# Kernel optimization log

Hardware: AMD Instinct MI355X
Metric: run time of the kernel (lower is better)

Reference implementation:

```python
import jax, jax.numpy as jnp
import numpy as np

B, S, H, D, M = 4, 512, 768, 24, 96
OUT_HID = 2 * max(128, H // 2)  # 768

def setup_inputs() -> dict:
    key = jax.random.key(0)
    ks = jax.random.split(key, 10)
    g = lambda k, shp, s=0.02: (jax.random.normal(k, shp, jnp.float32) * s)
    return {
        'H_j': jax.random.normal(ks[0], (B, S, H), jnp.float32),
        'H_i': jax.random.normal(ks[1], (B, S, H), jnp.float32),
        'attn_mask': jnp.ones((B, S), jnp.float32),
        'p_j_w': g(ks[2], (D, H)),
        'p_i_w': g(ks[3], (D, H)),
        's_w1': g(ks[4], (M, 4 * D)),
        's_b1': jnp.zeros((M,), jnp.float32),
        's_w2': g(ks[5], (1, M)),
        's_b2': jnp.zeros((1,), jnp.float32),
        'v_w1': g(ks[6], (OUT_HID, 3 * H)),
        'v_b1': jnp.zeros((OUT_HID,), jnp.float32),
        'v_w2': g(ks[7], (H, OUT_HID)),
        'v_b2': jnp.zeros((H,), jnp.float32),
        'alpha': jnp.asarray(0.05, jnp.float32),
    }

def reference(H_j, H_i, attn_mask, p_j_w, p_i_w, s_w1, s_b1, s_w2, s_b2,
              v_w1, v_b1, v_w2, v_b2, alpha):
    # Projections: [B,S,D]
    Zj = H_j @ p_j_w.T
    Zi = H_i @ p_i_w.T
    # score_mlp layer1 on concat([Zj_pair, Zi_pair, hadam, |diff|]) ==
    # sum of the 4 block-matmuls (block-split of W1 over the concat axis).
    Wa, Wb, Wc, Wd = jnp.split(s_w1, 4, axis=1)        # each [M, D]
    Zj_p = Zj[:, :, None, :]                            # [B,S,1,D]
    Zi_p = Zi[:, None, :, :]                            # [B,1,S,D]
    hid = (jnp.einsum('bsd,md->bsm', Zj, Wa)[:, :, None, :]
           + jnp.einsum('btd,md->btm', Zi, Wb)[:, None, :, :]
           + jnp.einsum('bstd,md->bstm', Zj_p * Zi_p, Wc)
           + jnp.einsum('bstd,md->bstm', jnp.abs(Zj_p - Zi_p), Wd)
           + s_b1)                                      # [B,S,S,M]
    logits = jnp.einsum('bstm,om->bst', jax.nn.relu(hid), s_w2)[..., :] + s_b2[0]  # [B,S,S]
    neg = jnp.finfo(logits.dtype).min
    logits = logits + (1.0 - attn_mask)[:, None, :] * neg  # mask over keys
    probs = jax.nn.softmax(logits, axis=-1)
    ctx = jnp.einsum('bst,bth->bsh', probs, H_i)           # [B,S,H]
    msg_in = jnp.concatenate([ctx, H_j, ctx * H_j], axis=-1)  # concat_hadam: [B,S,3H]
    msg = jax.nn.relu(msg_in @ v_w1.T + v_b1) @ v_w2.T + v_b2
    return alpha * msg  # dropout is identity in eval mode
```

## Files before the change

### kernel.cpp

```cpp
#include <hip/hip_runtime.h>
#include <hip/hip_bf16.h>
#include <math.h>

#define BB 4
#define SS 512
#define HH 768
#define DD 24
#define MM 96
#define OH 768
#define K3H 2304

typedef unsigned short u16;
typedef unsigned int u32;
typedef short bf16x8 __attribute__((ext_vector_type(8)));
typedef float f32x4 __attribute__((ext_vector_type(4)));
typedef u16 u16x4 __attribute__((ext_vector_type(4)));

#define MB_MSGIN  0
#define MB_H1     (MB_MSGIN + BB*SS*K3H)
#define MB_W1     (MB_H1    + BB*SS*OH)
#define MB_W2     (MB_W1    + OH*K3H)
#define MB_PROBS  (MB_W2    + OH*HH)
#define MB_HIT    (MB_PROBS + BB*SS*SS)
#define MB_ZJP    (MB_HIT   + BB*HH*SS)
#define MB_ZIP    (MB_ZJP   + BB*SS*32)
#define MB_WM     (MB_ZIP   + BB*SS*32)
#define MB_WAB    (MB_WM    + MM*96)
#define MB_AB     (MB_WAB   + MM*32)

__device__ inline u16 f2bf(float x) {
    union { float f; u32 u; } v; v.f = x;
    u32 r = v.u + 0x7fffu + ((v.u >> 16) & 1u);
    return (u16)(r >> 16);
}
__device__ inline u32 pk2bf(float lo, float hi) {
    return ((__float_as_uint(lo) + 0x8000u) >> 16) |
           ((__float_as_uint(hi) + 0x8000u) & 0xffff0000u);
}
__device__ inline void unpack8(bf16x8 v, float* f) {
    const u32* d = (const u32*)&v;
    #pragma unroll
    for (int i = 0; i < 4; ++i) {
        f[2*i]   = __uint_as_float(d[i] << 16);
        f[2*i+1] = __uint_as_float(d[i] & 0xffff0000u);
    }
}
__device__ inline void gl_lds16(const u16* g, u16* l) {
    __builtin_amdgcn_global_load_lds(
        (const __attribute__((address_space(1))) void*)g,
        (__attribute__((address_space(3))) void*)l, 16, 0, 0);
}
__device__ inline bf16x8 frag64(const u16* X, int r, int g) {
    return *(const bf16x8*)&X[(r*8 + (g ^ (r & 7)))*8];
}

__global__ __launch_bounds__(256) void k_wprep(
    const float* __restrict__ sw1, const float* __restrict__ vw1,
    const float* __restrict__ vw2,
    u16* __restrict__ Wm, u16* __restrict__ Wab,
    u16* __restrict__ w1b, u16* __restrict__ w2b)
{
    int bx = blockIdx.x;
    if (bx == 0) {
        for (int i = threadIdx.x; i < MM*96; i += 256) {
            int m = i / 96, k = i % 96;
            float v = 0.f;
            if (k < 24)                 v = sw1[m*96 + 48 + k];
            else if (k >= 32 && k < 56) v = sw1[m*96 + 72 + (k - 32)];
            else if (k >= 64 && k < 88) v = sw1[m*96 + 24 + (k - 64)];
            Wm[i] = f2bf(v);
        }
        for (int i = threadIdx.x; i < MM*32; i += 256) {
            int m = i >> 5, k = i & 31;
            Wab[i] = (k < 24) ? f2bf(sw1[m*96 + k]) : (u16)0;
        }
        return;
    }
    int idx = bx - 1;
    const float* src; u16* dst;
    if (idx < 864) { src = vw1; dst = w1b; }
    else           { idx -= 864; src = vw2; dst = w2b; }
    int i = (idx*256 + threadIdx.x) * 8;
    float4 a = *(const float4*)&src[i];
    float4 c = *(const float4*)&src[i+4];
    u16x4 lo = { f2bf(a.x), f2bf(a.y), f2bf(a.z), f2bf(a.w) };
    u16x4 hi = { f2bf(c.x), f2bf(c.y), f2bf(c.z), f2bf(c.w) };
    *(u16x4*)&dst[i]   = lo;
    *(u16x4*)&dst[i+4] = hi;
}

__global__ __launch_bounds__(256) void k_zgemm(
    const float* __restrict__ Hj, const float* __restrict__ Hi,
    const float* __restrict__ pjw, const float* __restrict__ piw,
    const float* __restrict__ sw1, const float* __restrict__ sb1,
    const u16* __restrict__ Wab,
    u16* __restrict__ Zjp, u16* __restrict__ Zip, u16* __restrict__ Ab)
{
    int isJ = (blockIdx.y == 0);
    const float* H = isJ ? Hj : Hi;
    const float* P = isJ ? pjw : piw;
    u16* Zout = isJ ? Zjp : Zip;
    int n0 = blockIdx.x * 64;
    int tid = threadIdx.x, wave = tid >> 6, lane = tid & 63;
    int q = lane >> 4, l16 = lane & 15;
    __shared__ __align__(16) u16 As[64*32];
    __shared__ __align__(16) u16 Bs[32*32];
    __shared__ __align__(16) u16 zb[64*32];

    { int i = tid; Bs[(24 + (i >> 5))*32 + (i & 31)] = 0; }

    int arow = tid >> 2, aseg = tid & 3;
    const float* ah = H + (size_t)(n0 + arow)*HH + aseg*8;
    int brow = tid >> 2, bseg = tid & 3;
    const float* bh = P + (size_t)brow*HH + bseg*8;
    int adst = arow*32 + ((aseg ^ (arow & 3))*8);
    int bdst = brow*32 + ((bseg ^ (brow & 3))*8);

    float4 xa = *(const float4*)(ah);
    float4 ya = *(const float4*)(ah + 4);
    float4 xb = {}, yb = {};
    if (tid < 96) { xb = *(const float4*)(bh); yb = *(const float4*)(bh + 4); }

    f32x4 acc0 = {}, acc1 = {};
    int ga = q ^ (l16 & 3);
    for (int k0 = 0; k0 < HH; k0 += 32) {
        { u32* w = (u32*)&As[adst];
          w[0] = pk2bf(xa.x, xa.y); w[1] = pk2bf(xa.z, xa.w);
          w[2] = pk2bf(ya.x, ya.y); w[3] = pk2bf(ya.z, ya.w); }
        if (tid < 96) {
          u32* w = (u32*)&Bs[bdst];
          w[0] = pk2bf(xb.x, xb.y); w[1] = pk2bf(xb.z, xb.w);
          w[2] = pk2bf(yb.x, yb.y); w[3] = pk2bf(yb.z, yb.w); }
        float4 nxa = {}, nya = {}, nxb = {}, nyb = {};
        if (k0 + 32 < HH) {
            nxa = *(const float4*)(ah + k0 + 32);
            nya = *(const float4*)(ah + k0 + 36);
            if (tid < 96) { nxb = *(const float4*)(bh + k0 + 32);
                            nyb = *(const float4*)(bh + k0 + 36); }
        }
        __syncthreads();
        bf16x8 af = *(const bf16x8*)&As[(wave*16 + l16)*32 + ga*8];
        bf16x8 b0 = *(const bf16x8*)&Bs[l16*32 + ga*8];
        bf16x8 b1 = *(const bf16x8*)&Bs[(16 + l16)*32 + ga*8];
        acc0 = __builtin_amdgcn_mfma_f32_16x16x32_bf16(af, b0, acc0, 0,0,0);
        acc1 = __builtin_amdgcn_mfma_f32_16x16x32_bf16(af, b1, acc1, 0,0,0);
        __syncthreads();
        xa = nxa; ya = nya; xb = nxb; yb = nyb;
    }
    #pragma unroll
    for (int r = 0; r < 4; ++r) {
        zb[(wave*16 + q*4 + r)*32 + l16]      = f2bf(acc0[r]);
        zb[(wave*16 + q*4 + r)*32 + 16 + l16] = f2bf(acc1[r]);
    }
    __syncthreads();
    { uint4 v = *(const uint4*)&zb[tid*8];
      *(uint4*)&Zout[(size_t)n0*32 + tid*8] = v; }
    if (isJ) {
        bf16x8 af = *(const bf16x8*)&zb[(wave*16 + l16)*32 + q*8];
        #pragma unroll
        for (int nt = 0; nt < 6; ++nt) {
            bf16x8 bw = *(const bf16x8*)&Wab[(nt*16 + l16)*32 + q*8];
            f32x4 a = {};
            a = __builtin_amdgcn_mfma_f32_16x16x32_bf16(af, bw, a, 0,0,0);
            float bv = sb1[nt*16 + l16];
            #pragma unroll
            for (int r = 0; r < 4; ++r) {
                int bs = n0 + wave*16 + q*4 + r;
                Ab[(size_t)bs*MM + nt*16 + l16] = f2bf(a[r] + bv);
            }
        }
    }
}

__global__ __launch_bounds__(256) void k_pair_mfma(
    const u16* __restrict__ Zjp, const u16* __restrict__ Zip,
    const u16* __restrict__ Ab, const u16* __restrict__ Wm,
    const float* __restrict__ sw2, const float* __restrict__ mask,
    u16* __restrict__ probsb)
{
    int blk = blockIdx.x; int b = blk >> 8; int s0 = (blk & 255) * 2;
    int tid = threadIdx.x, wave = tid >> 6, lane = tid & 63;
    int q = lane >> 4, l16 = lane & 15;
    int si = wave & 1, half = wave >> 1;
    int s = s0 + si, bs = b*SS + s;
    __shared__ __align__(16) u16 ZiS[SS*32];
    __shared__ float logits[2][SS];

    {
        const u16* zb = Zip + (size_t)b*SS*32;
        #pragma unroll
        for (int p = 0; p < 8; ++p) {
            int idx = p*256 + tid;
            int t = idx >> 2, c = idx & 3;
            int g = c ^ ((t + (t >> 2)) & 3);
            gl_lds16(zb + t*32 + g*8, ZiS + idx*8);
        }
    }

    bf16x8 zjf = *(const bf16x8*)&Zjp[(size_t)bs*32 + q*8];
    float zj[8]; unpack8(zjf, zj);
    bf16x8 afc[6], afd[6];
    #pragma unroll
    for (int mt = 0; mt < 6; ++mt) {
        const u16* wrow = &Wm[(mt*16 + l16)*96];
        bf16x8 wcf = *(const bf16x8*)&wrow[q*8];
        afd[mt]    = *(const bf16x8*)&wrow[32 + q*8];
        bf16x8 wbf = *(const bf16x8*)&wrow[64 + q*8];
        float fc[8], fb[8];
        unpack8(wcf, fc); unpack8(wbf, fb);
        u32 aval = (u32)Ab[(size_t)bs*MM + mt*16 + l16];
        union { u32 d[4]; bf16x8 v; } pk;
        #pragma unroll
        for (int i = 0; i < 4; ++i)
            pk.d[i] = pk2bf(fmaf(fc[2*i], zj[2*i], fb[2*i]),
                            fmaf(fc[2*i+1], zj[2*i+1], fb[2*i+1]));
        pk.d[0] = (q == 3) ? aval : pk.d[0];
        afc[mt] = pk.v;
    }
    float w2v[6][4];
    #pragma unroll
    for (int mt = 0; mt < 6; ++mt)
        #pragma unroll
        for (int r = 0; r < 4; ++r) w2v[mt][r] = sw2[mt*16 + q*4 + r];

    __syncthreads();

    for (int k = 0; k < 16; ++k) {
        int t0 = (half*16 + k) * 16;
        int trow = t0 + l16;
        int sw = q ^ ((trow + (trow >> 2)) & 3);
        bf16x8 zif = *(const bf16x8*)&ZiS[trow*32 + sw*8];
        float zi[8]; unpack8(zif, zi);
        union { u32 d[4]; bf16x8 v; } b1, b2;
        #pragma unroll
        for (int i = 0; i < 4; ++i)
            b1.d[i] = pk2bf(fabsf(zj[2*i] - zi[2*i]), fabsf(zj[2*i+1] - zi[2*i+1]));
        b2.v = zif;
        b2.d[0] = (q == 3) ? 0x3F80u : b2.d[0];
        f32x4 acc[6];
        #pragma unroll
        for (int mt = 0; mt < 6; ++mt) {
            f32x4 a = {};
            a = __builtin_amdgcn_mfma_f32_16x16x32_bf16(afc[mt], b2.v, a, 0,0,0);
            a = __builtin_amdgcn_mfma_f32_16x16x32_bf16(afd[mt], b1.v, a, 0,0,0);
            acc[mt] = a;
        }
        float p = 0.f;
        #pragma unroll
        for (int mt = 0; mt < 6; ++mt)
            #pragma unroll
            for (int r = 0; r < 4; ++r)
                p = fmaf(fmaxf(acc[mt][r], 0.f), w2v[mt][r], p);
        p += __shfl_xor(p, 16);
        p += __shfl_xor(p, 32);
        if (lane < 16) logits[si][t0 + lane] = p;
    }
    __syncthreads();

    if (wave < 2) {
        const float NEGF = -3.4028234663852886e38f;
        int bss = b*SS + s0 + wave;
        float l[8], e[8];
        float mx = -INFINITY;
        #pragma unroll
        for (int i = 0; i < 8; ++i) {
            int idx = lane + i*64;
            l[i] = logits[wave][idx] + (1.f - mask[b*SS + idx]) * NEGF;
            mx = fmaxf(mx, l[i]);
        }
        #pragma unroll
        for (int off = 32; off > 0; off >>= 1) mx = fmaxf(mx, __shfl_xor(mx, off));
        float sum = 0.f;
        #pragma unroll
        for (int i = 0; i < 8; ++i) { e[i] = __expf(l[i] - mx); sum += e[i]; }
        #pragma unroll
        for (int off = 32; off > 0; off >>= 1) sum += __shfl_xor(sum, off);
        float inv = 1.f / sum;
        #pragma unroll
        for (int i = 0; i < 8; ++i)
            probsb[(size_t)bss*SS + lane + i*64] = f2bf(e[i] * inv);
    }
}

__global__ __launch_bounds__(256) void k_hit(
    const float* __restrict__ Hi, u16* __restrict__ HiTb)
{
    int b = blockIdx.z, t0 = blockIdx.x*64, h0 = blockIdx.y*64;
    __shared__ u16 tile[64*74];
    int r = threadIdx.x >> 2, cs = threadIdx.x & 3;
    const float* src = Hi + ((size_t)(b*SS) + t0 + r)*HH + h0 + cs*16;
    u16* dst = &tile[r*74 + cs*16];
    #pragma unroll
    for (int i = 0; i < 4; ++i) {
        float4 v = *(const float4*)(src + i*4);
        *(u32*)&dst[i*4]     = pk2bf(v.x, v.y);
        *(u32*)&dst[i*4 + 2] = pk2bf(v.z, v.w);
    }
    __syncthreads();
    int hr = threadIdx.x >> 2;
    u16 outv[16];
    #pragma unroll
    for (int i = 0; i < 16; ++i) outv[i] = tile[(cs*16 + i)*74 + hr];
    u16* o = HiTb + ((size_t)b*HH + h0 + hr)*SS + t0 + cs*16;
    *(uint4*)o       = *(const uint4*)&outv[0];
    *(uint4*)(o + 8) = *(const uint4*)&outv[8];
}

__global__ __launch_bounds__(256) void k_ctx_mfma(
    const u16* __restrict__ probsb, const u16* __restrict__ HiTb,
    const float* __restrict__ Hj, u16* __restrict__ msginb)
{
    int b = blockIdx.z;
    int h0 = blockIdx.x * 64;
    int s0 = blockIdx.y * 64;
    int tid = threadIdx.x;
    __shared__ __align__(16) u16 As[64*64];
    __shared__ __align__(16) u16 Bs[64*64];
    int wave = tid >> 6, lane = tid & 63;
    int wr = (wave >> 1) * 32, wc = (wave & 1) * 32;
    int q = lane >> 4, l16 = lane & 15;
    f32x4 acc[2][2] = {};
    const u16* ag = probsb + ((size_t)(b*SS) + s0)*SS;
    const u16* bg = HiTb + ((size_t)b*HH + h0)*SS;
    for (int k0 = 0; k0 < SS; k0 += 64) {
        #pragma unroll
        for (int p = 0; p < 2; ++p) {
            int sl = p*256 + tid; int rr = sl >> 3, gi = sl & 7, g = gi ^ (rr & 7);
            gl_lds16(ag + (size_t)rr*SS + k0 + g*8, As + sl*8);
            gl_lds16(bg + (size_t)rr*SS + k0 + g*8, Bs + sl*8);
        }
        __syncthreads();
        #pragma unroll
        for (int ks = 0; ks < 2; ++ks) {
            int g = ks*4 + q;
            bf16x8 a0 = frag64(As, wr + l16, g);
            bf16x8 a1 = frag64(As, wr + 16 + l16, g);
            bf16x8 b0 = frag64(Bs, wc + l16, g);
            bf16x8 b1 = frag64(Bs, wc + 16 + l16, g);
            acc[0][0] = __builtin_amdgcn_mfma_f32_16x16x32_bf16(a0, b0, acc[0][0], 0,0,0);
            acc[0][1] = __builtin_amdgcn_mfma_f32_16x16x32_bf16(a0, b1, acc[0][1], 0,0,0);
            acc[1][0] = __builtin_amdgcn_mfma_f32_16x16x32_bf16(a1, b0, acc[1][0], 0,0,0);
            acc[1][1] = __builtin_amdgcn_mfma_f32_16x16x32_bf16(a1, b1, acc[1][1], 0,0,0);
        }
        __syncthreads();
    }
    #pragma unroll
    for (int rt = 0; rt < 2; ++rt) {
        #pragma unroll
        for (int ct = 0; ct < 2; ++ct) {
            int h = h0 + wc + ct*16 + l16;
            #pragma unroll
            for (int r = 0; r < 4; ++r) {
                int s = s0 + wr + rt*16 + q*4 + r;
                float v = acc[rt][ct][r];
                float hj = Hj[((size_t)(b*SS) + s)*HH + h];
                u16* mb = msginb + (size_t)(b*SS + s)*K3H + h;
                mb[0]    = f2bf(v);
                mb[HH]   = f2bf(hj);
                mb[2*HH] = f2bf(v * hj);
            }
        }
    }
}

__global__ __launch_bounds__(256) void k_mfma_gemm1(
    const u16* __restrict__ Abf, const u16* __restrict__ Bbf,
    const float* __restrict__ bias, u16* __restrict__ Cbf)
{
    int o0 = blockIdx.x * 64;
    int n0 = blockIdx.y * 64;
    int tid = threadIdx.x;
    __shared__ __align__(16) u16 As[64*64];
    __shared__ __align__(16) u16 Bs[64*64];
    int wave = tid >> 6, lane = tid & 63;
    int wr = (wave >> 1) * 32, wc = (wave & 1) * 32;
    int q = lane >> 4, l16 = lane & 15;
    f32x4 acc[2][2] = {};
    const u16* ag = Abf + (size_t)n0*K3H;
    const u16* bg = Bbf + (size_t)o0*K3H;
    for (int k0 = 0; k0 < K3H; k0 += 64) {
        #pragma unroll
        for (int p = 0; p < 2; ++p) {
            int sl = p*256 + tid; int rr = sl >> 3, gi = sl & 7, g = gi ^ (rr & 7);
            gl_lds16(ag + (size_t)rr*K3H + k0 + g*8, As + sl*8);
            gl_lds16(bg + (size_t)rr*K3H + k0 + g*8, Bs + sl*8);
        }
        __syncthreads();
        #pragma unroll
        for (int ks = 0; ks < 2; ++ks) {
            int g = ks*4 + q;
            bf16x8 a0 = frag64(As, wr + l16, g);
            bf16x8 a1 = frag64(As, wr + 16 + l16, g);
            bf16x8 b0 = frag64(Bs, wc + l16, g);
            bf16x8 b1 = frag64(Bs, wc + 16 + l16, g);
            acc[0][0] = __builtin_amdgcn_mfma_f32_16x16x32_bf16(a0, b0, acc[0][0], 0,0,0);
            acc[0][1] = __builtin_amdgcn_mfma_f32_16x16x32_bf16(a0, b1, acc[0][1], 0,0,0);
            acc[1][0] = __builtin_amdgcn_mfma_f32_16x16x32_bf16(a1, b0, acc[1][0], 0,0,0);
            acc[1][1] = __builtin_amdgcn_mfma_f32_16x16x32_bf16(a1, b1, acc[1][1], 0,0,0);
        }
        __syncthreads();
    }
    #pragma unroll
    for (int rt = 0; rt < 2; ++rt) {
        #pragma unroll
        for (int ct = 0; ct < 2; ++ct) {
            int o = o0 + wc + ct*16 + l16;
            float bv = bias[o];
            #pragma unroll
            for (int r = 0; r < 4; ++r) {
                int m = n0 + wr + rt*16 + q*4 + r;
                Cbf[(size_t)m*OH + o] = f2bf(fmaxf(acc[rt][ct][r] + bv, 0.f));
            }
        }
    }
}

__global__ __launch_bounds__(256) void k_mfma_gemm2(
    const u16* __restrict__ Abf, const u16* __restrict__ Bbf,
    const float* __restrict__ bias, const float* __restrict__ alpha,
    float* __restrict__ out)
{
    int o0 = blockIdx.x * 64;
    int n0 = blockIdx.y * 64;
    int tid = threadIdx.x;
    __shared__ __align__(16) u16 As[64*64];
    __shared__ __align__(16) u16 Bs[64*64];
    int wave = tid >> 6, lane = tid & 63;
    int wr = (wave >> 1) * 32, wc = (wave & 1) * 32;
    int q = lane >> 4, l16 = lane & 15;
    f32x4 acc[2][2] = {};
    const u16* ag = Abf + (size_t)n0*OH;
    const u16* bg = Bbf + (size_t)o0*OH;
    for (int k0 = 0; k0 < OH; k0 += 64) {
        #pragma unroll
        for (int p = 0; p < 2; ++p) {
            int sl = p*256 + tid; int rr = sl >> 3, gi = sl & 7, g = gi ^ (rr & 7);
            gl_lds16(ag + (size_t)rr*OH + k0 + g*8, As + sl*8);
            gl_lds16(bg + (size_t)rr*OH + k0 + g*8, Bs + sl*8);
        }
        __syncthreads();
        #pragma unroll
        for (int ks = 0; ks < 2; ++ks) {
            int g = ks*4 + q;
            bf16x8 a0 = frag64(As, wr + l16, g);
            bf16x8 a1 = frag64(As, wr + 16 + l16, g);
            bf16x8 b0 = frag64(Bs, wc + l16, g);
            bf16x8 b1 = frag64(Bs, wc + 16 + l16, g);
            acc[0][0] = __builtin_amdgcn_mfma_f32_16x16x32_bf16(a0, b0, acc[0][0], 0,0,0);
            acc[0][1] = __builtin_amdgcn_mfma_f32_16x16x32_bf16(a0, b1, acc[0][1], 0,0,0);
            acc[1][0] = __builtin_amdgcn_mfma_f32_16x16x32_bf16(a1, b0, acc[1][0], 0,0,0);
            acc[1][1] = __builtin_amdgcn_mfma_f32_16x16x32_bf16(a1, b1, acc[1][1], 0,0,0);
        }
        __syncthreads();
    }
    float al = alpha[0];
    #pragma unroll
    for (int rt = 0; rt < 2; ++rt) {
        #pragma unroll
        for (int ct = 0; ct < 2; ++ct) {
            int o = o0 + wc + ct*16 + l16;
            float bv = bias[o];
            #pragma unroll
            for (int r = 0; r < 4; ++r) {
                int m = n0 + wr + rt*16 + q*4 + r;
                out[(size_t)m*HH + o] = al * (acc[rt][ct][r] + bv);
            }
        }
    }
}

extern "C" void kernel_launch(void* const* d_in, const int* in_sizes, int n_in,
                              void* d_out, int out_size, void* d_ws, size_t ws_size,
                              hipStream_t stream) {
    const float* Hj    = (const float*)d_in[0];
    const float* Hi    = (const float*)d_in[1];
    const float* amask = (const float*)d_in[2];
    const float* pjw   = (const float*)d_in[3];
    const float* piw   = (const float*)d_in[4];
    const float* sw1   = (const float*)d_in[5];
    const float* sb1   = (const float*)d_in[6];
    const float* sw2   = (const float*)d_in[7];
    const float* sb2   = (const float*)d_in[8];
    const float* vw1   = (const float*)d_in[9];
    const float* vb1   = (const float*)d_in[10];
    const float* vw2   = (const float*)d_in[11];
    const float* vb2   = (const float*)d_in[12];
    const float* alpha = (const float*)d_in[13];
    float* out = (float*)d_out;
    (void)sb2;

    u16* bfbase = (u16*)d_ws;
    u16* msginb = bfbase + MB_MSGIN;
    u16* h1b    = bfbase + MB_H1;
    u16* w1b    = bfbase + MB_W1;
    u16* w2b    = bfbase + MB_W2;
    u16* probsb = bfbase + MB_PROBS;
    u16* hitb   = bfbase + MB_HIT;
    u16* zjp    = bfbase + MB_ZJP;
    u16* zip    = bfbase + MB_ZIP;
    u16* wm     = bfbase + MB_WM;
    u16* wab    = bfbase + MB_WAB;
    u16* ab     = bfbase + MB_AB;

    k_wprep<<<1 + 864 + 288, 256, 0, stream>>>(sw1, vw1, vw2, wm, wab, w1b, w2b);
    k_zgemm<<<dim3(32, 2), 256, 0, stream>>>(Hj, Hi, pjw, piw, sw1, sb1, wab, zjp, zip, ab);
    k_hit<<<dim3(SS/64, HH/64, BB), 256, 0, stream>>>(Hi, hitb);
    k_pair_mfma<<<BB*SS/2, 256, 0, stream>>>(zjp, zip, ab, wm, sw2, amask, probsb);
    k_ctx_mfma<<<dim3(HH/64, SS/64, BB), 256, 0, stream>>>(probsb, hitb, Hj, msginb);
    k_mfma_gemm1<<<dim3(OH/64, BB*SS/64), 256, 0, stream>>>(msginb, w1b, vb1, h1b);
    k_mfma_gemm2<<<dim3(HH/64, BB*SS/64), 256, 0, stream>>>(h1b, w2b, vb2, alpha, out);
}
```

Before: 194.5 us.

## Merge prep kernels into one launch and vectorize ctx epilogue via LDS staging

Merges the weight conversion, Z projection GEMM and Hi transpose into one block-indexed prep kernel. The prep kernel now also writes the bf16 copy of Hj into the middle slice of the message input. The context GEMM epilogue stages its accumulators through LDS and writes ctx and ctx*Hj as 16-byte vector stores, reading the bf16 Hj back instead of strided fp32 loads. This cuts kernel launches and scattered 2-byte stores. The product now uses bf16-rounded ctx and Hj, and the small Wm prep remains a separate single-block kernel.

```diff
diff --git a/kernel.cpp b/kernel.cpp
--- a/kernel.cpp
+++ b/kernel.cpp
@@ -54,121 +54,162 @@
     return *(const bf16x8*)&X[(r*8 + (g ^ (r & 7)))*8];
 }
 
-__global__ __launch_bounds__(256) void k_wprep(
-    const float* __restrict__ sw1, const float* __restrict__ vw1,
-    const float* __restrict__ vw2,
-    u16* __restrict__ Wm, u16* __restrict__ Wab,
-    u16* __restrict__ w1b, u16* __restrict__ w2b)
+__global__ __launch_bounds__(256) void k_wm(
+    const float* __restrict__ sw1, u16* __restrict__ Wm, u16* __restrict__ Wab)
 {
-    int bx = blockIdx.x;
-    if (bx == 0) {
-        for (int i = threadIdx.x; i < MM*96; i += 256) {
-            int m = i / 96, k = i % 96;
-            float v = 0.f;
-            if (k < 24)                 v = sw1[m*96 + 48 + k];
-            else if (k >= 32 && k < 56) v = sw1[m*96 + 72 + (k - 32)];
-            else if (k >= 64 && k < 88) v = sw1[m*96 + 24 + (k - 64)];
-            Wm[i] = f2bf(v);
-        }
-        for (int i = threadIdx.x; i < MM*32; i += 256) {
-            int m = i >> 5, k = i & 31;
-            Wab[i] = (k < 24) ? f2bf(sw1[m*96 + k]) : (u16)0;
-        }
-        return;
-    }
-    int idx = bx - 1;
-    const float* src; u16* dst;
-    if (idx < 864) { src = vw1; dst = w1b; }
-    else           { idx -= 864; src = vw2; dst = w2b; }
-    int i = (idx*256 + threadIdx.x) * 8;
-    float4 a = *(const float4*)&src[i];
-    float4 c = *(const float4*)&src[i+4];
-    u16x4 lo = { f2bf(a.x), f2bf(a.y), f2bf(a.z), f2bf(a.w) };
-    u16x4 hi = { f2bf(c.x), f2bf(c.y), f2bf(c.z), f2bf(c.w) };
-    *(u16x4*)&dst[i]   = lo;
-    *(u16x4*)&dst[i+4] = hi;
-}
-
-__global__ __launch_bounds__(256) void k_zgemm(
+    for (int i = threadIdx.x; i < MM*96; i += 256) {
+        int m = i / 96, k = i % 96;
+        float v = 0.f;
+        if (k < 24)                 v = sw1[m*96 + 48 + k];
+        else if (k >= 32 && k < 56) v = sw1[m*96 + 72 + (k - 32)];
+        else if (k >= 64 && k < 88) v = sw1[m*96 + 24 + (k - 64)];
+        Wm[i] = f2bf(v);
+    }
+    for (int i = threadIdx.x; i < MM*32; i += 256) {
+        int m = i >> 5, k = i & 31;
+        Wab[i] = (k < 24) ? f2bf(sw1[m*96 + k]) : (u16)0;
+    }
+}
+
+#define PZ_END   64
+#define PC1_END  928
+#define PC2_END  1216
+#define PHJ_END  1984
+#define PHT_END  2368
+
+__global__ __launch_bounds__(256) void k_prep(
     const float* __restrict__ Hj, const float* __restrict__ Hi,
     const float* __restrict__ pjw, const float* __restrict__ piw,
-    const float* __restrict__ sw1, const float* __restrict__ sb1,
+    const float* __restrict__ sb1,
+    const float* __restrict__ vw1, const float* __restrict__ vw2,
     const u16* __restrict__ Wab,
-    u16* __restrict__ Zjp, u16* __restrict__ Zip, u16* __restrict__ Ab)
+    u16* __restrict__ w1b, u16* __restrict__ w2b,
+    u16* __restrict__ Zjp, u16* __restrict__ Zip, u16* __restrict__ Ab,
+    u16* __restrict__ msginb, u16* __restrict__ HiTb)
 {
-    int isJ = (blockIdx.y == 0);
-    const float* H = isJ ? Hj : Hi;
-    const float* P = isJ ? pjw : piw;
-    u16* Zout = isJ ? Zjp : Zip;
-    int n0 = blockIdx.x * 64;
-    int tid = threadIdx.x, wave = tid >> 6, lane = tid & 63;
-    int q = lane >> 4, l16 = lane & 15;
-    __shared__ __align__(16) u16 As[64*32];
-    __shared__ __align__(16) u16 Bs[32*32];
-    __shared__ __align__(16) u16 zb[64*32];
-
-    { int i = tid; Bs[(24 + (i >> 5))*32 + (i & 31)] = 0; }
-
-    int arow = tid >> 2, aseg = tid & 3;
-    const float* ah = H + (size_t)(n0 + arow)*HH + aseg*8;
-    int brow = tid >> 2, bseg = tid & 3;
-    const float* bh = P + (size_t)brow*HH + bseg*8;
-    int adst = arow*32 + ((aseg ^ (arow & 3))*8);
-    int bdst = brow*32 + ((bseg ^ (brow & 3))*8);
-
-    float4 xa = *(const float4*)(ah);
-    float4 ya = *(const float4*)(ah + 4);
-    float4 xb = {}, yb = {};
-    if (tid < 96) { xb = *(const float4*)(bh); yb = *(const float4*)(bh + 4); }
-
-    f32x4 acc0 = {}, acc1 = {};
-    int ga = q ^ (l16 & 3);
-    for (int k0 = 0; k0 < HH; k0 += 32) {
-        { u32* w = (u32*)&As[adst];
-          w[0] = pk2bf(xa.x, xa.y); w[1] = pk2bf(xa.z, xa.w);
-          w[2] = pk2bf(ya.x, ya.y); w[3] = pk2bf(ya.z, ya.w); }
-        if (tid < 96) {
-          u32* w = (u32*)&Bs[bdst];
-          w[0] = pk2bf(xb.x, xb.y); w[1] = pk2bf(xb.z, xb.w);
-          w[2] = pk2bf(yb.x, yb.y); w[3] = pk2bf(yb.z, yb.w); }
-        float4 nxa = {}, nya = {}, nxb = {}, nyb = {};
-        if (k0 + 32 < HH) {
-            nxa = *(const float4*)(ah + k0 + 32);
-            nya = *(const float4*)(ah + k0 + 36);
-            if (tid < 96) { nxb = *(const float4*)(bh + k0 + 32);
-                            nyb = *(const float4*)(bh + k0 + 36); }
-        }
-        __syncthreads();
-        bf16x8 af = *(const bf16x8*)&As[(wave*16 + l16)*32 + ga*8];
-        bf16x8 b0 = *(const bf16x8*)&Bs[l16*32 + ga*8];
-        bf16x8 b1 = *(const bf16x8*)&Bs[(16 + l16)*32 + ga*8];
-        acc0 = __builtin_amdgcn_mfma_f32_16x16x32_bf16(af, b0, acc0, 0,0,0);
-        acc1 = __builtin_amdgcn_mfma_f32_16x16x32_bf16(af, b1, acc1, 0,0,0);
-        __syncthreads();
-        xa = nxa; ya = nya; xb = nxb; yb = nyb;
-    }
-    #pragma unroll
-    for (int r = 0; r < 4; ++r) {
-        zb[(wave*16 + q*4 + r)*32 + l16]      = f2bf(acc0[r]);
-        zb[(wave*16 + q*4 + r)*32 + 16 + l16] = f2bf(acc1[r]);
-    }
-    __syncthreads();
-    { uint4 v = *(const uint4*)&zb[tid*8];
-      *(uint4*)&Zout[(size_t)n0*32 + tid*8] = v; }
-    if (isJ) {
-        bf16x8 af = *(const bf16x8*)&zb[(wave*16 + l16)*32 + q*8];
-        #pragma unroll
-        for (int nt = 0; nt < 6; ++nt) {
-            bf16x8 bw = *(const bf16x8*)&Wab[(nt*16 + l16)*32 + q*8];
-            f32x4 a = {};
-            a = __builtin_amdgcn_mfma_f32_16x16x32_bf16(af, bw, a, 0,0,0);
-            float bv = sb1[nt*16 + l16];
+    __shared__ __align__(16) u16 smem[5120];
+    int bx = blockIdx.x;
+    int tid = threadIdx.x;
+
+    if (bx < PZ_END) {
+        int idx = bx;
+        int isJ = (idx < 32);
+        int n0 = (idx & 31) * 64;
+        const float* H = isJ ? Hj : Hi;
+        const float* P = isJ ? pjw : piw;
+        u16* Zout = isJ ? Zjp : Zip;
+        u16* As = smem;
+        u16* Bs = smem + 2048;
+        u16* zb = smem + 3072;
+        int wave = tid >> 6, lane = tid & 63;
+        int q = lane >> 4, l16 = lane & 15;
+
+        { int i = tid; Bs[(24 + (i >> 5))*32 + (i & 31)] = 0; }
+
+        int arow = tid >> 2, aseg = tid & 3;
+        const float* ah = H + (size_t)(n0 + arow)*HH + aseg*8;
+        const float* bh = P + (size_t)arow*HH + aseg*8;
+        int adst = arow*32 + ((aseg ^ (arow & 3))*8);
+
+        float4 xa = *(const float4*)(ah);
+        float4 ya = *(const float4*)(ah + 4);
+        float4 xb = {}, yb = {};
+        if (tid < 96) { xb = *(const float4*)(bh); yb = *(const float4*)(bh + 4); }
+
+        f32x4 acc0 = {}, acc1 = {};
+        int ga = q ^ (l16 & 3);
+        for (int k0 = 0; k0 < HH; k0 += 32) {
+            { u32* w = (u32*)&As[adst];
+              w[0] = pk2bf(xa.x, xa.y); w[1] = pk2bf(xa.z, xa.w);
+              w[2] = pk2bf(ya.x, ya.y); w[3] = pk2bf(ya.z, ya.w); }
+            if (tid < 96) {
+              u32* w = (u32*)&Bs[adst];
+              w[0] = pk2bf(xb.x, xb.y); w[1] = pk2bf(xb.z, xb.w);
+              w[2] = pk2bf(yb.x, yb.y); w[3] = pk2bf(yb.z, yb.w); }
+            float4 nxa = {}, nya = {}, nxb = {}, nyb = {};
+            if (k0 + 32 < HH) {
+                nxa = *(const float4*)(ah + k0 + 32);
+                nya = *(const float4*)(ah + k0 + 36);
+                if (tid < 96) { nxb = *(const float4*)(bh + k0 + 32);
+                                nyb = *(const float4*)(bh + k0 + 36); }
+            }
+            __syncthreads();
+            bf16x8 af = *(const bf16x8*)&As[(wave*16 + l16)*32 + ga*8];
+            bf16x8 b0 = *(const bf16x8*)&Bs[l16*32 + ga*8];
+            bf16x8 b1 = *(const bf16x8*)&Bs[(16 + l16)*32 + ga*8];
+            acc0 = __builtin_amdgcn_mfma_f32_16x16x32_bf16(af, b0, acc0, 0,0,0);
+            acc1 = __builtin_amdgcn_mfma_f32_16x16x32_bf16(af, b1, acc1, 0,0,0);
+            __syncthreads();
+            xa = nxa; ya = nya; xb = nxb; yb = nyb;
+        }
+        #pragma unroll
+        for (int r = 0; r < 4; ++r) {
+            zb[(wave*16 + q*4 + r)*32 + l16]      = f2bf(acc0[r]);
+            zb[(wave*16 + q*4 + r)*32 + 16 + l16] = f2bf(acc1[r]);
+        }
+        __syncthreads();
+        { uint4 v = *(const uint4*)&zb[tid*8];
+          *(uint4*)&Zout[(size_t)n0*32 + tid*8] = v; }
+        if (isJ) {
+            bf16x8 af = *(const bf16x8*)&zb[(wave*16 + l16)*32 + q*8];
             #pragma unroll
-            for (int r = 0; r < 4; ++r) {
-                int bs = n0 + wave*16 + q*4 + r;
-                Ab[(size_t)bs*MM + nt*16 + l16] = f2bf(a[r] + bv);
+            for (int nt = 0; nt < 6; ++nt) {
+                bf16x8 bw = *(const bf16x8*)&Wab[(nt*16 + l16)*32 + q*8];
+                f32x4 a = {};
+                a = __builtin_amdgcn_mfma_f32_16x16x32_bf16(af, bw, a, 0,0,0);
+                float bv = sb1[nt*16 + l16];
+                #pragma unroll
+                for (int r = 0; r < 4; ++r) {
+                    int bs = n0 + wave*16 + q*4 + r;
+                    Ab[(size_t)bs*MM + nt*16 + l16] = f2bf(a[r] + bv);
+                }
             }
         }
+    } else if (bx < PC2_END) {
+        int idx; const float* src; u16* dst;
+        if (bx < PC1_END) { idx = bx - PZ_END;  src = vw1; dst = w1b; }
+        else              { idx = bx - PC1_END; src = vw2; dst = w2b; }
+        int i = (idx*256 + tid) * 8;
+        float4 a = *(const float4*)&src[i];
+        float4 c = *(const float4*)&src[i+4];
+        u16x4 lo = { f2bf(a.x), f2bf(a.y), f2bf(a.z), f2bf(a.w) };
+        u16x4 hi = { f2bf(c.x), f2bf(c.y), f2bf(c.z), f2bf(c.w) };
+        *(u16x4*)&dst[i]   = lo;
+        *(u16x4*)&dst[i+4] = hi;
+    } else if (bx < PHJ_END) {
+        int idx = bx - PC2_END;
+        int e = (idx*256 + tid) * 8;
+        int n = e / HH, k = e - n*HH;
+        float4 a = *(const float4*)&Hj[e];
+        float4 c = *(const float4*)&Hj[e+4];
+        u16* dst = msginb + (size_t)n*K3H + HH + k;
+        u16x4 lo = { f2bf(a.x), f2bf(a.y), f2bf(a.z), f2bf(a.w) };
+        u16x4 hi = { f2bf(c.x), f2bf(c.y), f2bf(c.z), f2bf(c.w) };
+        *(u16x4*)&dst[0] = lo;
+        *(u16x4*)&dst[4] = hi;
+    } else {
+        int idx = bx - PHJ_END;
+        int t0 = (idx & 7) * 64;
+        int h0 = ((idx >> 3) % 12) * 64;
+        int b  = idx / 96;
+        u16* tile = smem;
+        int r = tid >> 2, cs = tid & 3;
+        const float* src = Hi + ((size_t)(b*SS) + t0 + r)*HH + h0 + cs*16;
+        u16* dst = &tile[r*74 + cs*16];
+        #pragma unroll
+        for (int i = 0; i < 4; ++i) {
+            float4 v = *(const float4*)(src + i*4);
+            *(u32*)&dst[i*4]     = pk2bf(v.x, v.y);
+            *(u32*)&dst[i*4 + 2] = pk2bf(v.z, v.w);
+        }
+        __syncthreads();
+        int hr = tid >> 2;
+        u16 outv[16];
+        #pragma unroll
+        for (int i = 0; i < 16; ++i) outv[i] = tile[(cs*16 + i)*74 + hr];
+        u16* o = HiTb + ((size_t)b*HH + h0 + hr)*SS + t0 + cs*16;
+        *(uint4*)o       = *(const uint4*)&outv[0];
+        *(uint4*)(o + 8) = *(const uint4*)&outv[8];
     }
 }
 
@@ -282,40 +323,17 @@
     }
 }
 
-__global__ __launch_bounds__(256) void k_hit(
-    const float* __restrict__ Hi, u16* __restrict__ HiTb)
-{
-    int b = blockIdx.z, t0 = blockIdx.x*64, h0 = blockIdx.y*64;
-    __shared__ u16 tile[64*74];
-    int r = threadIdx.x >> 2, cs = threadIdx.x & 3;
-    const float* src = Hi + ((size_t)(b*SS) + t0 + r)*HH + h0 + cs*16;
-    u16* dst = &tile[r*74 + cs*16];
-    #pragma unroll
-    for (int i = 0; i < 4; ++i) {
-        float4 v = *(const float4*)(src + i*4);
-        *(u32*)&dst[i*4]     = pk2bf(v.x, v.y);
-        *(u32*)&dst[i*4 + 2] = pk2bf(v.z, v.w);
-    }
-    __syncthreads();
-    int hr = threadIdx.x >> 2;
-    u16 outv[16];
-    #pragma unroll
-    for (int i = 0; i < 16; ++i) outv[i] = tile[(cs*16 + i)*74 + hr];
-    u16* o = HiTb + ((size_t)b*HH + h0 + hr)*SS + t0 + cs*16;
-    *(uint4*)o       = *(const uint4*)&outv[0];
-    *(uint4*)(o + 8) = *(const uint4*)&outv[8];
-}
-
 __global__ __launch_bounds__(256) void k_ctx_mfma(
     const u16* __restrict__ probsb, const u16* __restrict__ HiTb,
-    const float* __restrict__ Hj, u16* __restrict__ msginb)
+    u16* __restrict__ msginb)
 {
     int b = blockIdx.z;
     int h0 = blockIdx.x * 64;
     int s0 = blockIdx.y * 64;
     int tid = threadIdx.x;
-    __shared__ __align__(16) u16 As[64*64];
-    __shared__ __align__(16) u16 Bs[64*64];
+    __shared__ __align__(16) u16 smem[8192];
+    u16* As = smem;
+    u16* Bs = smem + 4096;
     int wave = tid >> 6, lane = tid & 63;
     int wr = (wave >> 1) * 32, wc = (wave & 1) * 32;
     int q = lane >> 4, l16 = lane & 15;
@@ -344,22 +362,39 @@
         }
         __syncthreads();
     }
+    u16* zb = smem;
     #pragma unroll
-    for (int rt = 0; rt < 2; ++rt) {
+    for (int rt = 0; rt < 2; ++rt)
         #pragma unroll
         for (int ct = 0; ct < 2; ++ct) {
-            int h = h0 + wc + ct*16 + l16;
+            int hl = wc + ct*16 + l16;
             #pragma unroll
-            for (int r = 0; r < 4; ++r) {
-                int s = s0 + wr + rt*16 + q*4 + r;
-                float v = acc[rt][ct][r];
-                float hj = Hj[((size_t)(b*SS) + s)*HH + h];
-                u16* mb = msginb + (size_t)(b*SS + s)*K3H + h;
-                mb[0]    = f2bf(v);
-                mb[HH]   = f2bf(hj);
-                mb[2*HH] = f2bf(v * hj);
-            }
-        }
+            for (int r = 0; r < 4; ++r)
+                zb[(wr + rt*16 + q*4 + r)*72 + hl] = f2bf(acc[rt][ct][r]);
+        }
+    __syncthreads();
+    {
+        int s_l = tid >> 2, seg = tid & 3;
+        u16 cv[16], hv[16], pv[16];
+        *(uint4*)&cv[0] = *(const uint4*)&zb[s_l*72 + seg*16];
+        *(uint4*)&cv[8] = *(const uint4*)&zb[s_l*72 + seg*16 + 8];
+        u16* row = msginb + (size_t)(b*SS + s0 + s_l)*K3H;
+        int hc = h0 + seg*16;
+        *(uint4*)&hv[0] = *(const uint4*)&row[HH + hc];
+        *(uint4*)&hv[8] = *(const uint4*)&row[HH + hc + 8];
+        #pragma unroll
+        for (int i = 0; i < 8; ++i) {
+            float c0 = __uint_as_float((u32)cv[2*i] << 16);
+            float c1 = __uint_as_float((u32)cv[2*i+1] << 16);
+            float g0 = __uint_as_float((u32)hv[2*i] << 16);
+            float g1 = __uint_as_float((u32)hv[2*i+1] << 16);
+            u32 pr = pk2bf(c0*g0, c1*g1);
+            pv[2*i] = (u16)pr; pv[2*i+1] = (u16)(pr >> 16);
+        }
+        *(uint4*)&row[hc]     = *(const uint4*)&cv[0];
+        *(uint4*)&row[hc + 8] = *(const uint4*)&cv[8];
+        *(uint4*)&row[2*HH + hc]     = *(const uint4*)&pv[0];
+        *(uint4*)&row[2*HH + hc + 8] = *(const uint4*)&pv[8];
     }
 }
 
@@ -502,11 +537,11 @@
     u16* wab    = bfbase + MB_WAB;
     u16* ab     = bfbase + MB_AB;
 
-    k_wprep<<<1 + 864 + 288, 256, 0, stream>>>(sw1, vw1, vw2, wm, wab, w1b, w2b);
-    k_zgemm<<<dim3(32, 2), 256, 0, stream>>>(Hj, Hi, pjw, piw, sw1, sb1, wab, zjp, zip, ab);
-    k_hit<<<dim3(SS/64, HH/64, BB), 256, 0, stream>>>(Hi, hitb);
+    k_wm<<<1, 256, 0, stream>>>(sw1, wm, wab);
+    k_prep<<<PHT_END, 256, 0, stream>>>(Hj, Hi, pjw, piw, sb1, vw1, vw2, wab,
+                                        w1b, w2b, zjp, zip, ab, msginb, hitb);
     k_pair_mfma<<<BB*SS/2, 256, 0, stream>>>(zjp, zip, ab, wm, sw2, amask, probsb);
-    k_ctx_mfma<<<dim3(HH/64, SS/64, BB), 256, 0, stream>>>(probsb, hitb, Hj, msginb);
+    k_ctx_mfma<<<dim3(HH/64, SS/64, BB), 256, 0, stream>>>(probsb, hitb, msginb);
     k_mfma_gemm1<<<dim3(OH/64, BB*SS/64), 256, 0, stream>>>(msginb, w1b, vb1, h1b);
     k_mfma_gemm2<<<dim3(HH/64, BB*SS/64), 256, 0, stream>>>(h1b, w2b, vb2, alpha, out);
 }
```

After: 191.0 us. Within noise of the previous version (-1.8%).
